# Optimization experiments

Measured on AMD Instinct MI355X. Metric: run time of the kernel, lower is better.

## Reference

```python
import jax, jax.numpy as jnp
import numpy as np

SCOPE = 27
IN_CHANNELS = 512
RICKER_WIDTH = 4.0
DAMP = 0.12
N, H, W = 16, 56, 56


def mexican_hat(scope, width, damping, self_connect=False):
    # Ricker (mexican hat) wavelet sampled at integer offsets around the center.
    t = jnp.arange(scope, dtype=jnp.float32) - (scope - 1) / 2.0
    norm = 2.0 / (np.sqrt(3.0 * width) * np.pi ** 0.25)
    w = damping * norm * (1.0 - (t / width) ** 2) * jnp.exp(-(t ** 2) / (2.0 * width ** 2))
    if not self_connect:
        w = w.at[scope // 2].set(0.0)  # zero self-connection at the center tap
    return w


def setup_inputs() -> dict:
    key = jax.random.key(0)
    activations = jax.random.normal(key, (N, IN_CHANNELS, H, W), dtype=jnp.float32)
    inhibition_filter = mexican_hat(SCOPE, RICKER_WIDTH, DAMP, self_connect=False)
    return {"activations": activations, "inhibition_filter": inhibition_filter}


def reference(activations, inhibition_filter):
    # Converged inhibition: solve y = x + k (circ-conv over channels) y, i.e.
    # y = F^-1( F(x) / F(delta - k_padded) ), FFT taken along the channel axis.
    C = activations.shape[1]
    scope = inhibition_filter.shape[0]
    # pad_roll: zero-pad the scope-length kernel to C taps, then roll so the
    # kernel center sits at circular position 0.
    k = jnp.pad(inhibition_filter, (0, C - scope))
    k = jnp.roll(k, -(scope // 2))
    delta = jnp.zeros((C,), dtype=activations.dtype).at[0].set(1.0)
    fk = jnp.fft.fft(delta - k)                      # complex [C]
    fx = jnp.fft.fft(activations, axis=1)            # complex [N,C,H,W]
    y = jnp.fft.ifft(fx / fk[None, :, None, None], axis=1).real
    return y.astype(activations.dtype)
```

## Files before the change

### kernel.cpp

```cpp
#include <hip/hip_runtime.h>
#include <cstdint>
#include <cstddef>

#define CCH   512
#define FSCOPE 27
#define HWSP  3136
#define NBATCH 16
#define NCOL  (NBATCH*HWSP)

#define BM 128
#define BN 128
#define BK 64
#define NKT (CCH/BK)

#define PI_F 3.14159265358979323846f

typedef __bf16 bf16x8 __attribute__((ext_vector_type(8)));
typedef float  f32x4  __attribute__((ext_vector_type(4)));

static __device__ __forceinline__ unsigned short f2bf(float f) {
  unsigned u = __builtin_bit_cast(unsigned, f);
  unsigned r = 0x7FFFu + ((u >> 16) & 1u);
  return (unsigned short)((u + r) >> 16);
}

__global__ __launch_bounds__(512)
void k_h2(const float* __restrict__ w, float* __restrict__ h) {
  __shared__ float red[8];
  const int d = blockIdx.x;
  const int m = threadIdx.x;

  float re = 1.0f, im = 0.0f;
  #pragma unroll
  for (int j = 0; j < FSCOPE; ++j) {
    int t = (m * (j - FSCOPE/2)) % CCH;
    if (t < 0) t += CCH;
    float ang = (2.0f * PI_F / CCH) * (float)t;
    float s, c;
    sincosf(ang, &s, &c);
    float wj = w[j];
    re -= wj * c;
    im += wj * s;
  }

  int t = (m * d) & (CCH - 1);
  float ang = (2.0f * PI_F / CCH) * (float)t;
  float s, c;
  sincosf(ang, &s, &c);
  float inv = 1.0f / (re * re + im * im);
  float term = (c * re + s * im) * inv;

  #pragma unroll
  for (int off = 32; off > 0; off >>= 1)
    term += __shfl_down(term, off, 64);

  const int lane = m & 63, wv = m >> 6;
  if (lane == 0) red[wv] = term;
  __syncthreads();
  if (m == 0) {
    float tot = 0.f;
    #pragma unroll
    for (int i = 0; i < 8; ++i) tot += red[i];
    h[d] = tot / (float)CCH;
  }
}

__global__ void k_buildH(const float* __restrict__ h, unsigned short* __restrict__ Hm) {
  int m = blockIdx.x;
  for (int k = threadIdx.x; k < CCH; k += blockDim.x) {
    Hm[m*CCH + k] = f2bf(h[(m - k) & (CCH - 1)]);
  }
}

__global__ __launch_bounds__(256)
void k_gemm(const float* __restrict__ X, const unsigned short* __restrict__ Hm,
            float* __restrict__ Y) {
  __shared__ __align__(16) unsigned char lds[49152];

  const int tid  = threadIdx.x;
  const int lane = tid & 63;
  const int w    = tid >> 6;

  int bid = blockIdx.x;
  int cpx = gridDim.x >> 3;
  int swz = (bid & 7) * cpx + (bid >> 3);
  const int tm = swz & 3;
  const int tc = swz >> 2;

  const int m0 = tm * BM;
  const int j0 = tc * BN;

  unsigned char* Bl = lds + 32768;

  const int fg = tid & 31;
  const int kg = tid >> 5;
  const int jb = j0 + fg*4;
  const int nb = jb / HWSP;
  const int sb = jb - nb * HWSP;
  const float* Xb = X + (size_t)nb * (CCH*(size_t)HWSP) + sb;

  int wrOff[4];
  #pragma unroll
  for (int c = 0; c < 4; ++c) {
    int col = fg*4 + c;
    int g = (col & 7) ^ ((col >> 3) & 7);
    wrOff[c] = col*128 + (((kg ^ g) & 7) << 4);
  }

  const int wr = w >> 1, wc = w & 1;
  int aBase[4], aSw[4], bBase[4], bSw[4];
  #pragma unroll
  for (int fm = 0; fm < 4; ++fm) {
    int m = wr*64 + fm*16 + (lane & 15);
    aBase[fm] = m*128;
    aSw[fm]   = (m & 7) << 4;
  }
  #pragma unroll
  for (int fn = 0; fn < 4; ++fn) {
    int col = wc*64 + fn*16 + (lane & 15);
    bBase[fn] = col*128;
    bSw[fn]   = ((col & 7) ^ ((col >> 3) & 7)) << 4;
  }

  const int aRow = lane >> 3;
  const int aChk = lane & 7;

  f32x4 acc[4][4];
  #pragma unroll
  for (int i = 0; i < 4; ++i)
    #pragma unroll
    for (int j = 0; j < 4; ++j)
      acc[i][j] = (f32x4){0.f, 0.f, 0.f, 0.f};

  float4 bv[8];

  #pragma unroll
  for (int i = 0; i < 4; ++i) {
    int m0w = w*32 + i*8;
    int m   = m0w + aRow;
    const unsigned short* src =
        Hm + (size_t)(m0 + m) * CCH + 8*(aChk ^ (m & 7));
    __builtin_amdgcn_global_load_lds(
        (const __attribute__((address_space(1))) void*)src,
        (__attribute__((address_space(3))) void*)(lds + m0w*128), 16, 0, 0);
  }
  #pragma unroll
  for (int kk = 0; kk < 8; ++kk)
    bv[kk] = *reinterpret_cast<const float4*>(Xb + (size_t)(kg*8 + kk) * HWSP);
  __syncthreads();
  #pragma unroll
  for (int c = 0; c < 4; ++c) {
    union { __bf16 h[8]; int4 v; } u;
    #pragma unroll
    for (int kk = 0; kk < 8; ++kk) {
      float f = (c==0) ? bv[kk].x : (c==1) ? bv[kk].y : (c==2) ? bv[kk].z : bv[kk].w;
      u.h[kk] = (__bf16)f;
    }
    *reinterpret_cast<int4*>(Bl + wrOff[c]) = u.v;
  }
  __syncthreads();

  for (int kt = 0; kt < NKT; ++kt) {
    const int aoffC = (kt & 1) * 16384;
    const int aoffN = 16384 - aoffC;

    if (kt + 1 < NKT) {
      #pragma unroll
      for (int i = 0; i < 4; ++i) {
        int m0w = w*32 + i*8;
        int m   = m0w + aRow;
        const unsigned short* src =
            Hm + (size_t)(m0 + m) * CCH + (kt + 1)*BK + 8*(aChk ^ (m & 7));
        __builtin_amdgcn_global_load_lds(
            (const __attribute__((address_space(1))) void*)src,
            (__attribute__((address_space(3))) void*)(lds + aoffN + m0w*128), 16, 0, 0);
      }
      const float* Xk = Xb + (size_t)((kt + 1)*BK + kg*8) * HWSP;
      #pragma unroll
      for (int kk = 0; kk < 8; ++kk)
        bv[kk] = *reinterpret_cast<const float4*>(Xk + (size_t)kk * HWSP);
    }

    #pragma unroll
    for (int ks = 0; ks < 2; ++ks) {
      const int kbyte = ks*64 + ((lane >> 4) << 4);
      bf16x8 af[4], bfr[4];
      #pragma unroll
      for (int fm = 0; fm < 4; ++fm)
        af[fm] = *reinterpret_cast<const bf16x8*>(lds + aoffC + aBase[fm] + (kbyte ^ aSw[fm]));
      #pragma unroll
      for (int fn = 0; fn < 4; ++fn)
        bfr[fn] = *reinterpret_cast<const bf16x8*>(Bl + bBase[fn] + (kbyte ^ bSw[fn]));
      #pragma unroll
      for (int fm = 0; fm < 4; ++fm)
        #pragma unroll
        for (int fn = 0; fn < 4; ++fn)
          acc[fm][fn] = __builtin_amdgcn_mfma_f32_16x16x32_bf16(
              af[fm], bfr[fn], acc[fm][fn], 0, 0, 0);
    }

    __syncthreads();

    if (kt + 1 < NKT) {
      #pragma unroll
      for (int c = 0; c < 4; ++c) {
        union { __bf16 h[8]; int4 v; } u;
        #pragma unroll
        for (int kk = 0; kk < 8; ++kk) {
          float f = (c==0) ? bv[kk].x : (c==1) ? bv[kk].y : (c==2) ? bv[kk].z : bv[kk].w;
          u.h[kk] = (__bf16)f;
        }
        *reinterpret_cast<int4*>(Bl + wrOff[c]) = u.v;
      }
      __syncthreads();
    }
  }

  #pragma unroll
  for (int fn = 0; fn < 4; ++fn) {
    int colg = j0 + wc*64 + fn*16 + (lane & 15);
    int n = colg / HWSP;
    int s = colg - n * HWSP;
    float* Yb = Y + (size_t)n * (CCH*(size_t)HWSP) + s;
    #pragma unroll
    for (int fm = 0; fm < 4; ++fm) {
      int mrow = m0 + wr*64 + fm*16 + ((lane >> 4) << 2);
      #pragma unroll
      for (int r = 0; r < 4; ++r)
        Yb[(size_t)(mrow + r) * HWSP] = acc[fm][fn][r];
    }
  }
}

extern "C" void kernel_launch(void* const* d_in, const int* in_sizes, int n_in,
                              void* d_out, int out_size, void* d_ws, size_t ws_size,
                              hipStream_t stream) {
  const float* X = (const float*)d_in[0];
  const float* w = (const float*)d_in[1];
  float* Y = (float*)d_out;

  float* h           = (float*)d_ws;
  unsigned short* Hm = (unsigned short*)((char*)d_ws + 4096);

  k_h2    <<<CCH, 512, 0, stream>>>(w, h);
  k_buildH<<<CCH, 256, 0, stream>>>(h, Hm);

  const int nblk = (CCH/BM) * (NCOL/BN);
  k_gemm  <<<nblk, 256, 0, stream>>>(X, Hm, Y);
}
```

Baseline: 59.91 us.

## Reshape GEMM tile to 256x64 so each block streams fewer X columns

Changes the GEMM block tile from 128x128 to 256x64 (M x columns), so only two M tiles cover the 512 channels and each activation column is read and converted to bf16 twice instead of four times. Each wave now owns 64 full rows and all 64 columns. X loads become scalar per-lane loads with 16 K-rows per wave instead of float4 loads. Block column offsets are computed once, relying on 64 dividing the 3136-column spatial size. The A tile double buffer grows to 64 KB, bringing LDS to 72 KB per block, which may lower occupancy.

```diff
diff --git a/kernel.cpp b/kernel.cpp
--- a/kernel.cpp
+++ b/kernel.cpp
@@ -8,8 +8,8 @@
 #define NBATCH 16
 #define NCOL  (NBATCH*HWSP)
 
-#define BM 128
-#define BN 128
+#define BM 256
+#define BN 64
 #define BK 64
 #define NKT (CCH/BK)
 
@@ -75,7 +75,7 @@
 __global__ __launch_bounds__(256)
 void k_gemm(const float* __restrict__ X, const unsigned short* __restrict__ Hm,
             float* __restrict__ Y) {
-  __shared__ __align__(16) unsigned char lds[49152];
+  __shared__ __align__(16) unsigned char lds[73728];
 
   const int tid  = threadIdx.x;
   const int lane = tid & 63;
@@ -84,40 +84,40 @@
   int bid = blockIdx.x;
   int cpx = gridDim.x >> 3;
   int swz = (bid & 7) * cpx + (bid >> 3);
-  const int tm = swz & 3;
-  const int tc = swz >> 2;
+  const int tm = swz & 1;
+  const int tc = swz >> 1;
 
   const int m0 = tm * BM;
   const int j0 = tc * BN;
-
-  unsigned char* Bl = lds + 32768;
-
-  const int fg = tid & 31;
-  const int kg = tid >> 5;
-  const int jb = j0 + fg*4;
-  const int nb = jb / HWSP;
-  const int sb = jb - nb * HWSP;
-  const float* Xb = X + (size_t)nb * (CCH*(size_t)HWSP) + sb;
-
-  int wrOff[4];
-  #pragma unroll
-  for (int c = 0; c < 4; ++c) {
-    int col = fg*4 + c;
-    int g = (col & 7) ^ ((col >> 3) & 7);
-    wrOff[c] = col*128 + (((kg ^ g) & 7) << 4);
-  }
-
-  const int wr = w >> 1, wc = w & 1;
+  const int nb = j0 / HWSP;
+  const int sb = j0 - nb * HWSP;
+  const float* Xblk = X + (size_t)nb * (CCH*(size_t)HWSP) + sb;
+  float*       Yblk = Y + (size_t)nb * (CCH*(size_t)HWSP) + sb;
+
+  unsigned char* Bl = lds + 65536;
+
+  const int fg = lane;
+  const int kg = w;
+  const float* Xcol = Xblk + fg;
+
+  int wrOff[2];
+  {
+    int g = (fg & 7) ^ ((fg >> 3) & 7);
+    #pragma unroll
+    for (int c = 0; c < 2; ++c)
+      wrOff[c] = fg*128 + ((((kg*2 + c) ^ g) & 7) << 4);
+  }
+
   int aBase[4], aSw[4], bBase[4], bSw[4];
   #pragma unroll
   for (int fm = 0; fm < 4; ++fm) {
-    int m = wr*64 + fm*16 + (lane & 15);
+    int m = w*64 + fm*16 + (lane & 15);
     aBase[fm] = m*128;
     aSw[fm]   = (m & 7) << 4;
   }
   #pragma unroll
   for (int fn = 0; fn < 4; ++fn) {
-    int col = wc*64 + fn*16 + (lane & 15);
+    int col = fn*16 + (lane & 15);
     bBase[fn] = col*128;
     bSw[fn]   = ((col & 7) ^ ((col >> 3) & 7)) << 4;
   }
@@ -132,11 +132,11 @@
     for (int j = 0; j < 4; ++j)
       acc[i][j] = (f32x4){0.f, 0.f, 0.f, 0.f};
 
-  float4 bv[8];
-
-  #pragma unroll
-  for (int i = 0; i < 4; ++i) {
-    int m0w = w*32 + i*8;
+  float bv[16];
+
+  #pragma unroll
+  for (int i = 0; i < 8; ++i) {
+    int m0w = w*64 + i*8;
     int m   = m0w + aRow;
     const unsigned short* src =
         Hm + (size_t)(m0 + m) * CCH + 8*(aChk ^ (m & 7));
@@ -145,29 +145,26 @@
         (__attribute__((address_space(3))) void*)(lds + m0w*128), 16, 0, 0);
   }
   #pragma unroll
-  for (int kk = 0; kk < 8; ++kk)
-    bv[kk] = *reinterpret_cast<const float4*>(Xb + (size_t)(kg*8 + kk) * HWSP);
+  for (int kk = 0; kk < 16; ++kk)
+    bv[kk] = Xcol[(size_t)(kg*16 + kk) * HWSP];
   __syncthreads();
   #pragma unroll
-  for (int c = 0; c < 4; ++c) {
+  for (int c = 0; c < 2; ++c) {
     union { __bf16 h[8]; int4 v; } u;
     #pragma unroll
-    for (int kk = 0; kk < 8; ++kk) {
-      float f = (c==0) ? bv[kk].x : (c==1) ? bv[kk].y : (c==2) ? bv[kk].z : bv[kk].w;
-      u.h[kk] = (__bf16)f;
-    }
+    for (int kk = 0; kk < 8; ++kk) u.h[kk] = (__bf16)bv[c*8 + kk];
     *reinterpret_cast<int4*>(Bl + wrOff[c]) = u.v;
   }
   __syncthreads();
 
   for (int kt = 0; kt < NKT; ++kt) {
-    const int aoffC = (kt & 1) * 16384;
-    const int aoffN = 16384 - aoffC;
+    const int aoffC = (kt & 1) * 32768;
+    const int aoffN = 32768 - aoffC;
 
     if (kt + 1 < NKT) {
       #pragma unroll
-      for (int i = 0; i < 4; ++i) {
-        int m0w = w*32 + i*8;
+      for (int i = 0; i < 8; ++i) {
+        int m0w = w*64 + i*8;
         int m   = m0w + aRow;
         const unsigned short* src =
             Hm + (size_t)(m0 + m) * CCH + (kt + 1)*BK + 8*(aChk ^ (m & 7));
@@ -175,10 +172,9 @@
             (const __attribute__((address_space(1))) void*)src,
             (__attribute__((address_space(3))) void*)(lds + aoffN + m0w*128), 16, 0, 0);
       }
-      const float* Xk = Xb + (size_t)((kt + 1)*BK + kg*8) * HWSP;
-      #pragma unroll
-      for (int kk = 0; kk < 8; ++kk)
-        bv[kk] = *reinterpret_cast<const float4*>(Xk + (size_t)kk * HWSP);
+      #pragma unroll
+      for (int kk = 0; kk < 16; ++kk)
+        bv[kk] = Xcol[(size_t)((kt + 1)*BK + kg*16 + kk) * HWSP];
     }
 
     #pragma unroll
@@ -203,13 +199,10 @@
 
     if (kt + 1 < NKT) {
       #pragma unroll
-      for (int c = 0; c < 4; ++c) {
+      for (int c = 0; c < 2; ++c) {
         union { __bf16 h[8]; int4 v; } u;
         #pragma unroll
-        for (int kk = 0; kk < 8; ++kk) {
-          float f = (c==0) ? bv[kk].x : (c==1) ? bv[kk].y : (c==2) ? bv[kk].z : bv[kk].w;
-          u.h[kk] = (__bf16)f;
-        }
+        for (int kk = 0; kk < 8; ++kk) u.h[kk] = (__bf16)bv[c*8 + kk];
         *reinterpret_cast<int4*>(Bl + wrOff[c]) = u.v;
       }
       __syncthreads();
@@ -218,16 +211,13 @@
 
   #pragma unroll
   for (int fn = 0; fn < 4; ++fn) {
-    int colg = j0 + wc*64 + fn*16 + (lane & 15);
-    int n = colg / HWSP;
-    int s = colg - n * HWSP;
-    float* Yb = Y + (size_t)n * (CCH*(size_t)HWSP) + s;
+    const int co = fn*16 + (lane & 15);
     #pragma unroll
     for (int fm = 0; fm < 4; ++fm) {
-      int mrow = m0 + wr*64 + fm*16 + ((lane >> 4) << 2);
+      int mrow = m0 + w*64 + fm*16 + ((lane >> 4) << 2);
       #pragma unroll
       for (int r = 0; r < 4; ++r)
-        Yb[(size_t)(mrow + r) * HWSP] = acc[fm][fn][r];
+        Yblk[(size_t)(mrow + r) * HWSP + co] = acc[fm][fn][r];
     }
   }
 }
```

Measured after the change: 67.21 us. +12.2%, slower.
